# Kernel optimization log

Hardware: AMD Instinct MI355X
Metric: run time of the kernel (lower is better)

Reference implementation:

```python
import jax, jax.numpy as jnp
import numpy as np

B, S, HID = 2, 2048, 4096
NH, NKV = 32, 8
HD = HID // NH          # 128
GROUPS = NH // NKV      # 4


def rotate_half(x):
    x1, x2 = x[..., : x.shape[-1] // 2], x[..., x.shape[-1] // 2 :]
    return jnp.concatenate((-x2, x1), axis=-1)


def apply_rope(x, cos, sin):
    # x: (B,H,S,D); cos/sin: (B,S,D) -> (B,1,S,D)
    c = cos[:, None, :, :]
    s = sin[:, None, :, :]
    return x * c + rotate_half(x) * s


def setup_inputs() -> dict:
    key = jax.random.key(0)
    ks = jax.random.split(key, 12)
    scale = 1.0 / np.sqrt(HID)
    return {
        "hidden_states": jax.random.normal(ks[0], (B, S, HID), jnp.float32),
        "cos": jax.random.uniform(ks[1], (B, S, HD), jnp.float32),
        "sin": jax.random.uniform(ks[2], (B, S, HD), jnp.float32),
        "Wq": jax.random.normal(ks[3], (HID, NH * HD), jnp.float32) * scale,
        "bq": jax.random.normal(ks[4], (NH * HD,), jnp.float32) * 0.01,
        "Wk": jax.random.normal(ks[5], (HID, NKV * HD), jnp.float32) * scale,
        "bk": jax.random.normal(ks[6], (NKV * HD,), jnp.float32) * 0.01,
        "Wv": jax.random.normal(ks[7], (HID, NKV * HD), jnp.float32) * scale,
        "bv": jax.random.normal(ks[8], (NKV * HD,), jnp.float32) * 0.01,
        "Wo": jax.random.normal(ks[9], (NH * HD, HID), jnp.float32) * scale,
    }


def reference(hidden_states, cos, sin, Wq, bq, Wk, bk, Wv, bv, Wo):
    b, s, _ = hidden_states.shape
    q = (hidden_states @ Wq + bq).reshape(b, s, NH, HD).transpose(0, 2, 1, 3)
    k = (hidden_states @ Wk + bk).reshape(b, s, NKV, HD).transpose(0, 2, 1, 3)
    v = (hidden_states @ Wv + bv).reshape(b, s, NKV, HD).transpose(0, 2, 1, 3)
    q = apply_rope(q, cos, sin)
    k = apply_rope(k, cos, sin)
    # GQA: repeat_interleave along head dim
    k = jnp.repeat(k, GROUPS, axis=1)
    v = jnp.repeat(v, GROUPS, axis=1)
    scores = jnp.einsum("bhqd,bhkd->bhqk", q, k) / np.sqrt(HD).astype(np.float32)
    weights = jax.nn.softmax(scores, axis=-1)  # NOTE: no causal mask, per source
    out = jnp.einsum("bhqk,bhkd->bhqd", weights, v)
    out = out.transpose(0, 2, 1, 3).reshape(b, s, NH * HD)
    return out @ Wo
```

## Files before the change

### kernel.cpp

```cpp
#include <hip/hip_runtime.h>
#include <stdint.h>

#define Bz   2
#define Ss   2048
#define HID  4096
#define NH   32
#define NKV  8
#define HD   128
#define Mrows (Bz*Ss)
#define NQKV 6144

typedef __attribute__((ext_vector_type(8))) short b16x8;
typedef __attribute__((ext_vector_type(8))) _Float16 f16x8;
typedef __attribute__((ext_vector_type(4))) float f32x4;

__device__ __forceinline__ unsigned short f2bf(float f) {
  union { float f; uint32_t u; } v; v.f = f;
  uint32_t r = v.u + 0x7FFFu + ((v.u >> 16) & 1u);
  return (unsigned short)(r >> 16);
}

__device__ __forceinline__ void cp16(const void* g, void* l) {
  __builtin_amdgcn_global_load_lds(
      (const __attribute__((address_space(1))) void*)g,
      (__attribute__((address_space(3))) void*)l, 16, 0, 0);
}

__global__ __launch_bounds__(256) void cast_x(const float* __restrict__ x,
                                              unsigned short* __restrict__ o) {
  int i = blockIdx.x*256 + threadIdx.x;
  float4 v = ((const float4*)x)[i];
  ushort4 r; r.x = f2bf(v.x); r.y = f2bf(v.y); r.z = f2bf(v.z); r.w = f2bf(v.w);
  ((ushort4*)o)[i] = r;
}

__global__ __launch_bounds__(256) void wtrans(const float* __restrict__ W,
                                              unsigned short* __restrict__ Wt,
                                              int K, int N) {
  __shared__ float t[32][33];
  int n0 = blockIdx.x*32, k0 = blockIdx.y*32;
  int tx = threadIdx.x & 31, ty = threadIdx.x >> 5;
#pragma unroll
  for (int i = 0; i < 4; i++)
    t[ty + i*8][tx] = W[(size_t)(k0 + ty + i*8)*N + n0 + tx];
  __syncthreads();
#pragma unroll
  for (int i = 0; i < 4; i++)
    Wt[(size_t)(n0 + ty + i*8)*K + k0 + tx] = f2bf(t[tx][ty + i*8]);
}

__global__ __launch_bounds__(256) void bias_cat(const float* __restrict__ bq,
                                                const float* __restrict__ bk,
                                                const float* __restrict__ bv,
                                                float* __restrict__ o) {
  int i = blockIdx.x*256 + threadIdx.x;
  float v = (i < 4096) ? bq[i] : (i < 5120) ? bk[i-4096] : bv[i-5120];
  o[i] = v;
}

__global__ __launch_bounds__(512, 2) void gemm_bt(const unsigned short* __restrict__ A,
                                                  const unsigned short* __restrict__ Bt,
                                                  const float* __restrict__ bias,
                                                  float* __restrict__ C,
                                                  int N, int K) {
  __shared__ short Al[2][256*64];
  __shared__ short Bl[2][256*64];
  const int tid = threadIdx.x;
  const int w = tid >> 6, lane = tid & 63;
  const int wm = w >> 2, wn = w & 3;
  const int lrow = lane & 15, quad = lane >> 4;
  const int swz = lrow & 7;
  int bid = blockIdx.y * gridDim.x + blockIdx.x;
  const int nwg = gridDim.x * gridDim.y;
  bid = (bid & 7) * (nwg >> 3) + (bid >> 3);
  const int m0 = (bid / gridDim.x) * 256;
  const int n0 = (bid % gridDim.x) * 256;
  const int rr = tid >> 3;
  const int gc = (tid & 7) ^ (rr & 7);
  const unsigned short* ga = A  + (size_t)(m0 + rr)*K + gc*8;
  const unsigned short* gb = Bt + (size_t)(n0 + rr)*K + gc*8;
  short* la = &Al[0][0] + (size_t)w*512;
  short* lb = &Bl[0][0] + (size_t)w*512;
  const short* arow = &Al[0][0] + (wm*128 + lrow)*64;
  const short* brow = &Bl[0][0] + (wn*64  + lrow)*64;
  const int kc = (quad ^ swz) * 8;
  const int NT = K >> 6;
  f32x4 acc[8][4] = {};

#define STAGE_T(buf, kt)                                                        \
  {                                                                             \
    _Pragma("unroll")                                                           \
    for (int j = 0; j < 4; j++) {                                               \
      cp16(ga + (size_t)(j*64)*K + (size_t)(kt)*64, la + (buf)*16384 + j*4096); \
      cp16(gb + (size_t)(j*64)*K + (size_t)(kt)*64, lb + (buf)*16384 + j*4096); \
    }                                                                           \
  }

  STAGE_T(0, 0);
  STAGE_T(1, 1);
  asm volatile("s_waitcnt vmcnt(8)" ::: "memory");
  __builtin_amdgcn_s_barrier();
  __builtin_amdgcn_sched_barrier(0);

  for (int t = 0; t < NT; ++t) {
    const int cb = (t & 1) * 16384;
    b16x8 af[8], bfr[4];
#pragma unroll
    for (int mi = 0; mi < 8; mi++)
      af[mi] = *(const b16x8*)(arow + cb + mi*1024 + kc);
#pragma unroll
    for (int ni = 0; ni < 4; ni++)
      bfr[ni] = *(const b16x8*)(brow + cb + ni*1024 + kc);
    __builtin_amdgcn_s_setprio(1);
#pragma unroll
    for (int mi = 0; mi < 8; mi++)
#pragma unroll
      for (int ni = 0; ni < 4; ni++)
        acc[mi][ni] = __builtin_amdgcn_mfma_f32_16x16x32_bf16(af[mi], bfr[ni], acc[mi][ni], 0, 0, 0);
    __builtin_amdgcn_s_setprio(0);
    b16x8 af1[8], bf1[4];
#pragma unroll
    for (int mi = 0; mi < 8; mi++)
      af1[mi] = *(const b16x8*)(arow + cb + mi*1024 + (kc ^ 32));
#pragma unroll
    for (int ni = 0; ni < 4; ni++)
      bf1[ni] = *(const b16x8*)(brow + cb + ni*1024 + (kc ^ 32));
    asm volatile("s_waitcnt lgkmcnt(0)" ::: "memory");
    __builtin_amdgcn_s_barrier();
    __builtin_amdgcn_sched_barrier(0);
    if (t + 2 < NT) STAGE_T(t & 1, t + 2);
    __builtin_amdgcn_sched_barrier(0);
    __builtin_amdgcn_s_setprio(1);
#pragma unroll
    for (int mi = 0; mi < 8; mi++)
#pragma unroll
      for (int ni = 0; ni < 4; ni++)
        acc[mi][ni] = __builtin_amdgcn_mfma_f32_16x16x32_bf16(af1[mi], bf1[ni], acc[mi][ni], 0, 0, 0);
    __builtin_amdgcn_s_setprio(0);
    if (t + 2 < NT) { asm volatile("s_waitcnt vmcnt(8)" ::: "memory"); }
    else            { asm volatile("s_waitcnt vmcnt(0)" ::: "memory"); }
    __builtin_amdgcn_s_barrier();
    __builtin_amdgcn_sched_barrier(0);
  }
#undef STAGE_T

#pragma unroll
  for (int mi = 0; mi < 8; mi++)
#pragma unroll
    for (int ni = 0; ni < 4; ni++) {
      int col = n0 + wn*64 + ni*16 + lrow;
      float bv = bias ? bias[col] : 0.0f;
#pragma unroll
      for (int r = 0; r < 4; r++) {
        int row = m0 + wm*128 + mi*16 + quad*4 + r;
        C[(size_t)row*N + col] = acc[mi][ni][r] + bv;
      }
    }
}

__global__ __launch_bounds__(256) void rope(const float* __restrict__ X, int xstride, int colbase,
                                            const float* __restrict__ cp,
                                            const float* __restrict__ sp,
                                            unsigned short* __restrict__ o, int nh, float scale) {
  int tid = blockIdx.x*256 + threadIdx.x;
  int d = tid & 63;
  int h = (tid >> 6) % nh;
  int m = tid / (64*nh);
  int b = m >> 11, s = m & 2047;
  size_t xoff = (size_t)m*xstride + colbase + (size_t)h*HD + d;
  float x1 = X[xoff], x2 = X[xoff + 64];
  const float* cb = cp + ((size_t)b*Ss + s)*HD;
  const float* sb = sp + ((size_t)b*Ss + s)*HD;
  float o1 = (x1*cb[d]      - x2*sb[d])      * scale;
  float o2 = (x2*cb[d + 64] + x1*sb[d + 64]) * scale;
  unsigned short* ob = o + ((size_t)(b*nh + h)*Ss + s)*HD;
  ob[d]      = f2bf(o1);
  ob[d + 64] = f2bf(o2);
}

__global__ __launch_bounds__(256) void vprep(const float* __restrict__ Vf, int xstride, int colbase,
                                             _Float16* __restrict__ Vt) {
  __shared__ float t[32][33];
  int dt = blockIdx.x, st = blockIdx.y, bk = blockIdx.z;
  int b = bk >> 3, kvh = bk & 7;
  int tx = threadIdx.x & 31, ty = threadIdx.x >> 5;
#pragma unroll
  for (int i = 0; i < 4; i++) {
    int s = st*32 + ty + i*8;
    t[ty + i*8][tx] = Vf[(size_t)(b*Ss + s)*xstride + colbase + kvh*HD + dt*32 + tx];
  }
  __syncthreads();
#pragma unroll
  for (int i = 0; i < 4; i++) {
    int d = dt*32 + ty + i*8;
    Vt[((size_t)bk*HD + d)*Ss + st*32 + tx] = (_Float16)t[tx][ty + i*8];
  }
}

__global__ __launch_bounds__(256) void flash(const unsigned short* __restrict__ Qr,
                                             const unsigned short* __restrict__ Kr,
                                             const _Float16* __restrict__ Vt,
                                             unsigned short* __restrict__ AO) {
  __shared__ short Kl[64*128];
  __shared__ short Vl[144*64];
  __shared__ _Float16 Pl[4][16*72];
  const int qt = blockIdx.x, h = blockIdx.y, b = blockIdx.z;
  const int tid = threadIdx.x, w = tid >> 6, lane = tid & 63;
  const int lrow = lane & 15, quad = lane >> 4;
  const int wb = tid & 192;
  const int swz = lrow & 7;
  const int kvh = h >> 2;
  const unsigned short* Qb = Qr + ((size_t)(b*NH + h)*Ss + qt*64 + w*16)*HD;
  const unsigned short* Kb = Kr + ((size_t)(b*NKV + kvh)*Ss)*HD;
  const _Float16*       Vb = Vt + ((size_t)(b*NKV + kvh)*HD)*Ss;
  {
    int idx = tid*4;
    int row = 128 + (idx >> 6);
    unsigned short v = (row == 128) ? 0x3C00u : 0u;
    ushort4 vv; vv.x = v; vv.y = v; vv.z = v; vv.w = v;
    *(ushort4*)((unsigned short*)Vl + 128*64 + idx) = vv;
  }
  b16x8 qf[4];
#pragma unroll
  for (int t = 0; t < 4; t++)
    qf[t] = *(const b16x8*)(Qb + (size_t)lrow*HD + t*32 + quad*8);
  f32x4 o[8] = {};
  f32x4 ol = {};
  for (int kt = 0; kt < 32; kt++) {
    __syncthreads();
#pragma unroll
    for (int i = 0; i < 4; i++) {
      int c = i*256 + tid;
      int r = c >> 4, gc = (c & 15) ^ (r & 7);
      cp16(Kb + (size_t)(kt*64 + r)*HD + gc*8, Kl + (i*256 + wb)*8);
    }
#pragma unroll
    for (int i = 0; i < 4; i++) {
      int c = i*256 + tid;
      int r = c >> 3, gc = (c & 7) ^ (r & 7);
      cp16(Vb + (size_t)r*Ss + kt*64 + gc*8, Vl + (i*256 + wb)*8);
    }
    __syncthreads();
    f32x4 sc[4] = {};
#pragma unroll
    for (int t = 0; t < 4; t++)
#pragma unroll
      for (int n = 0; n < 4; n++) {
        b16x8 kf = *(const b16x8*)(Kl + (n*16 + lrow)*128 + ((t*4 + quad) ^ swz)*8);
        sc[n] = __builtin_amdgcn_mfma_f32_16x16x32_bf16(qf[t], kf, sc[n], 0, 0, 0);
      }
#pragma unroll
    for (int n = 0; n < 4; n++)
#pragma unroll
      for (int r = 0; r < 4; r++)
        Pl[w][(quad*4 + r)*72 + n*16 + lrow] = (_Float16)__builtin_amdgcn_exp2f(sc[n][r]);
#pragma unroll
    for (int st = 0; st < 2; st++) {
      f16x8 pf = *(const f16x8*)(&Pl[w][lrow*72 + st*32 + quad*8]);
#pragma unroll
      for (int n = 0; n < 8; n++) {
        f16x8 vf = *(const f16x8*)((const _Float16*)Vl + (n*16 + lrow)*64 + ((st*4 + quad) ^ swz)*8);
        o[n] = __builtin_amdgcn_mfma_f32_16x16x32_f16(pf, vf, o[n], 0, 0, 0);
      }
      f16x8 vf1 = *(const f16x8*)((const _Float16*)Vl + (128 + lrow)*64 + ((st*4 + quad) ^ swz)*8);
      ol = __builtin_amdgcn_mfma_f32_16x16x32_f16(pf, vf1, ol, 0, 0, 0);
    }
  }
  float rl[4];
#pragma unroll
  for (int r = 0; r < 4; r++)
    rl[r] = 1.0f / __shfl(ol[r], lane & 48);
  const int s0 = qt*64 + w*16;
#pragma unroll
  for (int n = 0; n < 8; n++)
#pragma unroll
    for (int r = 0; r < 4; r++) {
      int srow = s0 + quad*4 + r;
      float v = o[n][r] * rl[r];
      AO[((size_t)(b*Ss + srow))*HID + h*HD + n*16 + lrow] = f2bf(v);
    }
}

extern "C" void kernel_launch(void* const* d_in, const int* in_sizes, int n_in,
                              void* d_out, int out_size, void* d_ws, size_t ws_size,
                              hipStream_t stream) {
  (void)in_sizes; (void)n_in; (void)out_size; (void)ws_size;
  const float* hs   = (const float*)d_in[0];
  const float* cosp = (const float*)d_in[1];
  const float* sinp = (const float*)d_in[2];
  const float* Wq   = (const float*)d_in[3];
  const float* bq   = (const float*)d_in[4];
  const float* Wk   = (const float*)d_in[5];
  const float* bk   = (const float*)d_in[6];
  const float* Wv   = (const float*)d_in[7];
  const float* bv   = (const float*)d_in[8];
  const float* Wo   = (const float*)d_in[9];
  float* out = (float*)d_out;
  const float QSC = 0.12751742826919558f;

  char* p = (char*)d_ws;
  unsigned short* Xb   = (unsigned short*)p; p += (size_t)Mrows*HID*2;
  unsigned short* Wcat = (unsigned short*)p; p += (size_t)NQKV*HID*2;
  unsigned short* Wot  = (unsigned short*)p; p += (size_t)HID*HID*2;
  float* bcat = (float*)p; p += (size_t)NQKV*4;
  float* QKVf = (float*)p; p += (size_t)Mrows*NQKV*4;
  unsigned short* Qr = Xb;
  unsigned short* Kr = Wcat;
  _Float16*       Vt = (_Float16*)(Wcat + (size_t)(Bz*NKV)*Ss*HD);
  unsigned short* AO = (unsigned short*)QKVf;

  cast_x<<<Mrows*HID/1024, 256, 0, stream>>>(hs, Xb);
  wtrans<<<dim3(HID/32, HID/32),      256, 0, stream>>>(Wq, Wcat,                        HID, HID);
  wtrans<<<dim3((NKV*HD)/32, HID/32), 256, 0, stream>>>(Wk, Wcat + (size_t)4096*HID,     HID, NKV*HD);
  wtrans<<<dim3((NKV*HD)/32, HID/32), 256, 0, stream>>>(Wv, Wcat + (size_t)5120*HID,     HID, NKV*HD);
  wtrans<<<dim3(HID/32, HID/32),      256, 0, stream>>>(Wo, Wot, HID, HID);
  bias_cat<<<NQKV/256, 256, 0, stream>>>(bq, bk, bv, bcat);

  gemm_bt<<<dim3(NQKV/256, Mrows/256), 512, 0, stream>>>(Xb, Wcat, bcat, QKVf, NQKV, HID);

  rope<<<(Mrows*NH*64)/256,  256, 0, stream>>>(QKVf, NQKV, 0,    cosp, sinp, Qr, NH,  QSC);
  rope<<<(Mrows*NKV*64)/256, 256, 0, stream>>>(QKVf, NQKV, 4096, cosp, sinp, Kr, NKV, 1.0f);
  vprep<<<dim3(HD/32, Ss/32, Bz*NKV), 256, 0, stream>>>(QKVf, NQKV, 5120, Vt);

  flash<<<dim3(Ss/64, NH, Bz), 256, 0, stream>>>(Qr, Kr, Vt, AO);

  gemm_bt<<<dim3(HID/256, Mrows/256), 512, 0, stream>>>(AO, Wot, nullptr, out, HID, HID);
}
```

Before: 864.1 us.

## Restructure GEMM main loop into four quadrant phases with interleaved async loads

```diff
diff --git a/kernel.cpp b/kernel.cpp
--- a/kernel.cpp
+++ b/kernel.cpp
@@ -63,8 +63,8 @@
                                                   const float* __restrict__ bias,
                                                   float* __restrict__ C,
                                                   int N, int K) {
-  __shared__ short Al[2][256*64];
-  __shared__ short Bl[2][256*64];
+  __shared__ __align__(16) short Al[2*16384];
+  __shared__ __align__(16) short Bl[2*16384];
   const int tid = threadIdx.x;
   const int w = tid >> 6, lane = tid & 63;
   const int wm = w >> 2, wn = w & 3;
@@ -75,74 +75,126 @@
   bid = (bid & 7) * (nwg >> 3) + (bid >> 3);
   const int m0 = (bid / gridDim.x) * 256;
   const int n0 = (bid % gridDim.x) * 256;
-  const int rr = tid >> 3;
-  const int gc = (tid & 7) ^ (rr & 7);
-  const unsigned short* ga = A  + (size_t)(m0 + rr)*K + gc*8;
-  const unsigned short* gb = Bt + (size_t)(n0 + rr)*K + gc*8;
-  short* la = &Al[0][0] + (size_t)w*512;
-  short* lb = &Bl[0][0] + (size_t)w*512;
-  const short* arow = &Al[0][0] + (wm*128 + lrow)*64;
-  const short* brow = &Bl[0][0] + (wn*64  + lrow)*64;
-  const int kc = (quad ^ swz) * 8;
+  const int srA = (tid >> 3) & 63;
+  const int srB = (tid >> 3) & 31;
+  const int gcA = (tid & 7) ^ (srA & 7);
+  const int gcB = (tid & 7) ^ (srB & 7);
+  const unsigned short* gaA = A  + (size_t)(m0 + srA)*K + gcA*8;
+  const unsigned short* gaB = Bt + (size_t)(n0 + (tid >> 8)*64 + srB)*K + gcB*8;
+  const int wbs = w*512;
+
+#define SB0() __builtin_amdgcn_sched_barrier(0)
+#define STAGE_A(buf, t, h) do {                                                         \
+    cp16(gaA + (size_t)((h)*64      )*K + (size_t)(t)*64, Al + (buf)*16384 + (h)*8192        + wbs); \
+    cp16(gaA + (size_t)((h)*64 + 128)*K + (size_t)(t)*64, Al + (buf)*16384 + (h)*8192 + 4096 + wbs); \
+  } while (0)
+#define STAGE_B(buf, t, h) do {                                                         \
+    cp16(gaB + (size_t)((h)*32      )*K + (size_t)(t)*64, Bl + (buf)*16384 + (h)*8192        + wbs); \
+    cp16(gaB + (size_t)((h)*32 + 128)*K + (size_t)(t)*64, Bl + (buf)*16384 + (h)*8192 + 4096 + wbs); \
+  } while (0)
+
+  const short* Ar = Al + wm*4096 + lrow*64;
+  const short* Br = Bl + wn*2048 + lrow*64;
+  const int kc0 = (quad ^ swz) * 8;
   const int NT = K >> 6;
   f32x4 acc[8][4] = {};
 
-#define STAGE_T(buf, kt)                                                        \
-  {                                                                             \
-    _Pragma("unroll")                                                           \
-    for (int j = 0; j < 4; j++) {                                               \
-      cp16(ga + (size_t)(j*64)*K + (size_t)(kt)*64, la + (buf)*16384 + j*4096); \
-      cp16(gb + (size_t)(j*64)*K + (size_t)(kt)*64, lb + (buf)*16384 + j*4096); \
-    }                                                                           \
-  }
-
-  STAGE_T(0, 0);
-  STAGE_T(1, 1);
-  asm volatile("s_waitcnt vmcnt(8)" ::: "memory");
+  STAGE_A(0, 0, 0); SB0(); STAGE_B(0, 0, 0); SB0();
+  STAGE_B(0, 0, 1); SB0(); STAGE_A(0, 0, 1); SB0();
+  if (NT > 1) { STAGE_A(1, 1, 0); SB0(); STAGE_B(1, 1, 0); SB0(); STAGE_B(1, 1, 1); SB0(); }
+  if (NT > 1) { asm volatile("s_waitcnt vmcnt(6)" ::: "memory"); }
+  else        { asm volatile("s_waitcnt vmcnt(0)" ::: "memory"); }
   __builtin_amdgcn_s_barrier();
-  __builtin_amdgcn_sched_barrier(0);
+  SB0();
 
   for (int t = 0; t < NT; ++t) {
     const int cb = (t & 1) * 16384;
-    b16x8 af[8], bfr[4];
-#pragma unroll
-    for (int mi = 0; mi < 8; mi++)
-      af[mi] = *(const b16x8*)(arow + cb + mi*1024 + kc);
-#pragma unroll
-    for (int ni = 0; ni < 4; ni++)
-      bfr[ni] = *(const b16x8*)(brow + cb + ni*1024 + kc);
+    b16x8 a0[4][2], a1[4][2], b0[2][2], b1[2][2];
+#pragma unroll
+    for (int mi = 0; mi < 4; mi++) {
+      a0[mi][0] = *(const b16x8*)(Ar + cb + mi*1024 + kc0);
+      a0[mi][1] = *(const b16x8*)(Ar + cb + mi*1024 + (kc0 ^ 32));
+    }
+#pragma unroll
+    for (int ni = 0; ni < 2; ni++) {
+      b0[ni][0] = *(const b16x8*)(Br + cb + ni*1024 + kc0);
+      b0[ni][1] = *(const b16x8*)(Br + cb + ni*1024 + (kc0 ^ 32));
+    }
+    if (t + 1 < NT) STAGE_A((t + 1) & 1, t + 1, 1);
+    __builtin_amdgcn_s_barrier();
+    asm volatile("s_waitcnt lgkmcnt(0)" ::: "memory");
+    SB0();
     __builtin_amdgcn_s_setprio(1);
 #pragma unroll
-    for (int mi = 0; mi < 8; mi++)
-#pragma unroll
-      for (int ni = 0; ni < 4; ni++)
-        acc[mi][ni] = __builtin_amdgcn_mfma_f32_16x16x32_bf16(af[mi], bfr[ni], acc[mi][ni], 0, 0, 0);
+    for (int mi = 0; mi < 4; mi++)
+#pragma unroll
+      for (int ni = 0; ni < 2; ni++) {
+        acc[mi][ni] = __builtin_amdgcn_mfma_f32_16x16x32_bf16(a0[mi][0], b0[ni][0], acc[mi][ni], 0, 0, 0);
+        acc[mi][ni] = __builtin_amdgcn_mfma_f32_16x16x32_bf16(a0[mi][1], b0[ni][1], acc[mi][ni], 0, 0, 0);
+      }
     __builtin_amdgcn_s_setprio(0);
-    b16x8 af1[8], bf1[4];
-#pragma unroll
-    for (int mi = 0; mi < 8; mi++)
-      af1[mi] = *(const b16x8*)(arow + cb + mi*1024 + (kc ^ 32));
-#pragma unroll
-    for (int ni = 0; ni < 4; ni++)
-      bf1[ni] = *(const b16x8*)(brow + cb + ni*1024 + (kc ^ 32));
+    __builtin_amdgcn_s_barrier();
+#pragma unroll
+    for (int ni = 0; ni < 2; ni++) {
+      b1[ni][0] = *(const b16x8*)(Br + cb + 8192 + ni*1024 + kc0);
+      b1[ni][1] = *(const b16x8*)(Br + cb + 8192 + ni*1024 + (kc0 ^ 32));
+    }
+    if (t + 2 < NT) STAGE_A(t & 1, t + 2, 0);
+    __builtin_amdgcn_s_barrier();
     asm volatile("s_waitcnt lgkmcnt(0)" ::: "memory");
-    __builtin_amdgcn_s_barrier();
-    __builtin_amdgcn_sched_barrier(0);
-    if (t + 2 < NT) STAGE_T(t & 1, t + 2);
-    __builtin_amdgcn_sched_barrier(0);
+    SB0();
     __builtin_amdgcn_s_setprio(1);
 #pragma unroll
-    for (int mi = 0; mi < 8; mi++)
-#pragma unroll
-      for (int ni = 0; ni < 4; ni++)
-        acc[mi][ni] = __builtin_amdgcn_mfma_f32_16x16x32_bf16(af1[mi], bf1[ni], acc[mi][ni], 0, 0, 0);
+    for (int mi = 0; mi < 4; mi++)
+#pragma unroll
+      for (int ni = 0; ni < 2; ni++) {
+        acc[mi][ni+2] = __builtin_amdgcn_mfma_f32_16x16x32_bf16(a0[mi][0], b1[ni][0], acc[mi][ni+2], 0, 0, 0);
+        acc[mi][ni+2] = __builtin_amdgcn_mfma_f32_16x16x32_bf16(a0[mi][1], b1[ni][1], acc[mi][ni+2], 0, 0, 0);
+      }
     __builtin_amdgcn_s_setprio(0);
-    if (t + 2 < NT) { asm volatile("s_waitcnt vmcnt(8)" ::: "memory"); }
-    else            { asm volatile("s_waitcnt vmcnt(0)" ::: "memory"); }
-    __builtin_amdgcn_s_barrier();
-    __builtin_amdgcn_sched_barrier(0);
-  }
-#undef STAGE_T
+    __builtin_amdgcn_s_barrier();
+#pragma unroll
+    for (int mi = 0; mi < 4; mi++) {
+      a1[mi][0] = *(const b16x8*)(Ar + cb + 8192 + mi*1024 + kc0);
+      a1[mi][1] = *(const b16x8*)(Ar + cb + 8192 + mi*1024 + (kc0 ^ 32));
+    }
+    if (t + 2 < NT) STAGE_B(t & 1, t + 2, 0);
+    __builtin_amdgcn_s_barrier();
+    asm volatile("s_waitcnt lgkmcnt(0)" ::: "memory");
+    SB0();
+    __builtin_amdgcn_s_setprio(1);
+#pragma unroll
+    for (int mi = 0; mi < 4; mi++)
+#pragma unroll
+      for (int ni = 0; ni < 2; ni++) {
+        acc[mi+4][ni] = __builtin_amdgcn_mfma_f32_16x16x32_bf16(a1[mi][0], b0[ni][0], acc[mi+4][ni], 0, 0, 0);
+        acc[mi+4][ni] = __builtin_amdgcn_mfma_f32_16x16x32_bf16(a1[mi][1], b0[ni][1], acc[mi+4][ni], 0, 0, 0);
+      }
+    __builtin_amdgcn_s_setprio(0);
+    __builtin_amdgcn_s_barrier();
+    if (t + 2 < NT) {
+      STAGE_B(t & 1, t + 2, 1);
+      asm volatile("s_waitcnt vmcnt(6)" ::: "memory");
+    } else {
+      asm volatile("s_waitcnt vmcnt(0)" ::: "memory");
+    }
+    __builtin_amdgcn_s_barrier();
+    SB0();
+    __builtin_amdgcn_s_setprio(1);
+#pragma unroll
+    for (int mi = 0; mi < 4; mi++)
+#pragma unroll
+      for (int ni = 0; ni < 2; ni++) {
+        acc[mi+4][ni+2] = __builtin_amdgcn_mfma_f32_16x16x32_bf16(a1[mi][0], b1[ni][0], acc[mi+4][ni+2], 0, 0, 0);
+        acc[mi+4][ni+2] = __builtin_amdgcn_mfma_f32_16x16x32_bf16(a1[mi][1], b1[ni][1], acc[mi+4][ni+2], 0, 0, 0);
+      }
+    __builtin_amdgcn_s_setprio(0);
+    __builtin_amdgcn_s_barrier();
+    SB0();
+  }
+#undef STAGE_A
+#undef STAGE_B
+#undef SB0
 
 #pragma unroll
   for (int mi = 0; mi < 8; mi++)
```

Result: faster. 840.8 us (-2.7%).
